# Optimization experiments

Hardware: AMD Instinct MI355X
Metric: run time of the kernel (lower is better)

Reference implementation:

```python
import jax, jax.numpy as jnp
import numpy as np

N_NODES = 50000
N_EDGES = 800000
IN_C, HID_C, OUT_C = 128, 96, 64
BN_EPS = 1e-5


def setup_inputs() -> dict:
    key = jax.random.key(0)
    ks = jax.random.split(key, 12)
    x = jax.random.normal(ks[0], (N_NODES, IN_C), dtype=jnp.float32)
    edge_weight = jax.random.uniform(ks[1], (N_EDGES,), dtype=jnp.float32)
    row = jax.random.randint(ks[2], (N_EDGES,), 0, N_NODES, dtype=jnp.int32)
    col = jax.random.randint(ks[3], (N_EDGES,), 0, N_NODES, dtype=jnp.int32)
    s = 0.05
    W1 = jax.random.normal(ks[4], (IN_C, HID_C), dtype=jnp.float32) * s
    b1 = jnp.zeros((HID_C,), dtype=jnp.float32)
    W2 = jax.random.normal(ks[5], (HID_C, HID_C), dtype=jnp.float32) * s
    b2 = jnp.zeros((HID_C,), dtype=jnp.float32)
    W3 = jax.random.normal(ks[6], (HID_C, OUT_C), dtype=jnp.float32) * s
    b3 = jnp.zeros((OUT_C,), dtype=jnp.float32)
    g1 = jnp.ones((HID_C,), dtype=jnp.float32)
    be1 = jnp.zeros((HID_C,), dtype=jnp.float32)
    g2 = jnp.ones((HID_C,), dtype=jnp.float32)
    be2 = jnp.zeros((HID_C,), dtype=jnp.float32)
    return {"x": x, "edge_weight": edge_weight, "row": row, "col": col,
            "W1": W1, "b1": b1, "W2": W2, "b2": b2, "W3": W3, "b3": b3,
            "g1": g1, "be1": be1, "g2": g2, "be2": be2}


def _gcn_conv(h, edge_weight, row, col, W, b):
    # GCNConv: adj_norm @ (h @ W) + b, adj in COO with normalized edge_weight
    h = h @ W  # [N, d_out]
    msg = edge_weight[:, None] * h[col]  # gather + scale: [E, d_out]
    agg = jax.ops.segment_sum(msg, row, num_segments=N_NODES)  # scatter-add
    return agg + b


def _batch_norm(h, gamma, beta):
    # BatchNorm1d (training-mode batch statistics, biased variance)
    mean = jnp.mean(h, axis=0)
    var = jnp.var(h, axis=0)
    return (h - mean) * jax.lax.rsqrt(var + BN_EPS) * gamma + beta


def reference(x, edge_weight, row, col, W1, b1, W2, b2, W3, b3, g1, be1, g2, be2):
    h = _gcn_conv(x, edge_weight, row, col, W1, b1)
    h = jax.nn.relu(_batch_norm(h, g1, be1))  # dropout is identity in eval
    h = _gcn_conv(h, edge_weight, row, col, W2, b2)
    h = jax.nn.relu(_batch_norm(h, g2, be2))
    h = _gcn_conv(h, edge_weight, row, col, W3, b3)
    return jax.nn.log_softmax(h, axis=-1)
```

## Files before the change

kernel.cpp:

```cpp
#include <hip/hip_runtime.h>
#include <hip/hip_bf16.h>
#include <math.h>

#define N_NODES 50000
#define N_EDGES 800000
#define IN_C 128
#define HID_C 96
#define OUT_C 64
#define BN_EPS 1e-5f

#define ELL_SHIFT 6
#define ELL_CAP   64

#define NGRP 8
#define GRP_ROWS ((N_NODES + NGRP - 1) / NGRP)

#define EW_SCALE 65535.0f
#define EW_INV   (1.0f / 65535.0f)

#define ST_SLICES 4

typedef __attribute__((ext_vector_type(8))) short short8;
typedef __attribute__((ext_vector_type(4))) float f32x4;

static __device__ __forceinline__ unsigned short f2b(float f) {
    __hip_bfloat16 b = __float2bfloat16(f);
    return *reinterpret_cast<unsigned short*>(&b);
}
static __device__ __forceinline__ float b2f(unsigned short u) {
    return __uint_as_float((unsigned)u << 16);
}
static __device__ __forceinline__ unsigned pack2(float a, float b) {
    return (unsigned)f2b(a) | ((unsigned)f2b(b) << 16);
}

#define FMA8(B, V, W)                                          \
    acc[(B) + 0] += (W) * __uint_as_float((V).x << 16);        \
    acc[(B) + 1] += (W) * __uint_as_float((V).x & 0xffff0000u);\
    acc[(B) + 2] += (W) * __uint_as_float((V).y << 16);        \
    acc[(B) + 3] += (W) * __uint_as_float((V).y & 0xffff0000u);\
    acc[(B) + 4] += (W) * __uint_as_float((V).z << 16);        \
    acc[(B) + 5] += (W) * __uint_as_float((V).z & 0xffff0000u);\
    acc[(B) + 6] += (W) * __uint_as_float((V).w << 16);        \
    acc[(B) + 7] += (W) * __uint_as_float((V).w & 0xffff0000u);

#define FMA4(B, V, W)                                          \
    acc[(B) + 0] += (W) * __uint_as_float((V).x << 16);        \
    acc[(B) + 1] += (W) * __uint_as_float((V).x & 0xffff0000u);\
    acc[(B) + 2] += (W) * __uint_as_float((V).y << 16);        \
    acc[(B) + 3] += (W) * __uint_as_float((V).y & 0xffff0000u);

__global__ void prep_all(const float* __restrict__ W1, const float* __restrict__ W2,
                         const float* __restrict__ W3,
                         unsigned short* __restrict__ Wt1,
                         unsigned short* __restrict__ Wt2,
                         unsigned short* __restrict__ Wt3,
                         int* __restrict__ cnt, float* __restrict__ stats) {
    int i = blockIdx.x * blockDim.x + threadIdx.x;
    const int n1 = IN_C * HID_C, n2 = HID_C * HID_C, n3 = HID_C * OUT_C;
    if (i < n1) {
        int j = i / IN_C, k = i % IN_C;
        Wt1[i] = f2b(W1[k * HID_C + j]);
    } else if (i < n1 + n2) {
        int t = i - n1, j = t / HID_C, k = t % HID_C;
        Wt2[t] = f2b(W2[k * HID_C + j]);
    } else if (i < n1 + n2 + n3) {
        int t = i - n1 - n2, j = t / HID_C, k = t % HID_C;
        Wt3[t] = f2b(W3[k * OUT_C + j]);
    }
    if (i < N_NODES) cnt[i] = 0;
    if (i < 2 * ST_SLICES * 2 * HID_C) stats[i] = 0.f;
}

__global__ __launch_bounds__(256)
void fill_ell(const int* __restrict__ row, const int* __restrict__ col,
              const float* __restrict__ ew, int* __restrict__ cnt,
              unsigned int* __restrict__ pairs) {
    int g = blockIdx.x & (NGRP - 1);
    int e = (blockIdx.x >> 3) * 256 + threadIdx.x;
    if (e >= N_EDGES) return;
    int r = row[e];
    int lo = g * GRP_ROWS;
    if ((unsigned)(r - lo) >= (unsigned)GRP_ROWS) return;
    int slot = atomicAdd(&cnt[r], 1);
    if (slot < ELL_CAP) {
        unsigned wq = (unsigned)(ew[e] * EW_SCALE + 0.5f);
        pairs[((size_t)r << ELL_SHIFT) + slot] = (wq << 16) | (unsigned)col[e];
    }
}

template <int K, int J, bool APPLY, bool XBF16>
__global__ __launch_bounds__(256)
void gemm_mfma(const void* __restrict__ xin,
               const unsigned short* __restrict__ Wt,
               const float* __restrict__ stats,
               const float* __restrict__ gamma,
               const float* __restrict__ beta,
               unsigned short* __restrict__ h, int N) {
    constexpr int MT = 64;
    constexpr int SK = K + 8;
    constexpr int NT = J / 16;
    __shared__ unsigned short Xs[MT * SK];
    __shared__ unsigned short Ws[J * SK];
    __shared__ float scsh_s[APPLY ? 2 * K : 2];

    int tid = threadIdx.x;
    int tileBase = blockIdx.x * MT;

    if (APPLY) {
        if (tid < K) {
            float s = 0.f, sq = 0.f;
#pragma unroll
            for (int sl = 0; sl < ST_SLICES; ++sl) {
                s  += stats[sl * 2 * K + tid];
                sq += stats[sl * 2 * K + K + tid];
            }
            const float invN = 1.f / N_NODES;
            float mean = s * invN;
            float var = sq * invN - mean * mean;
            float sc = gamma[tid] * rsqrtf(var + BN_EPS);
            scsh_s[tid] = sc;
            scsh_s[K + tid] = beta[tid] - mean * sc;
        }
        __syncthreads();
    }

    if (XBF16) {
        const unsigned short* xb = (const unsigned short*)xin;
        for (int i = tid; i < MT * (K / 8); i += 256) {
            int node = i / (K / 8), kq = i % (K / 8);
            int gn = min(tileBase + node, N - 1);
            const unsigned short* src = xb + (size_t)gn * K + kq * 8;
            ushort4 u0 = *(const ushort4*)(src);
            ushort4 u1 = *(const ushort4*)(src + 4);
            if (APPLY) {
                int kb = kq * 8;
                float v0 = fmaxf(b2f(u0.x) * scsh_s[kb + 0] + scsh_s[K + kb + 0], 0.f);
                float v1 = fmaxf(b2f(u0.y) * scsh_s[kb + 1] + scsh_s[K + kb + 1], 0.f);
                float v2 = fmaxf(b2f(u0.z) * scsh_s[kb + 2] + scsh_s[K + kb + 2], 0.f);
                float v3 = fmaxf(b2f(u0.w) * scsh_s[kb + 3] + scsh_s[K + kb + 3], 0.f);
                float v4 = fmaxf(b2f(u1.x) * scsh_s[kb + 4] + scsh_s[K + kb + 4], 0.f);
                float v5 = fmaxf(b2f(u1.y) * scsh_s[kb + 5] + scsh_s[K + kb + 5], 0.f);
                float v6 = fmaxf(b2f(u1.z) * scsh_s[kb + 6] + scsh_s[K + kb + 6], 0.f);
                float v7 = fmaxf(b2f(u1.w) * scsh_s[kb + 7] + scsh_s[K + kb + 7], 0.f);
                u0 = make_ushort4(f2b(v0), f2b(v1), f2b(v2), f2b(v3));
                u1 = make_ushort4(f2b(v4), f2b(v5), f2b(v6), f2b(v7));
            }
            *(ushort4*)&Xs[node * SK + kq * 8] = u0;
            *(ushort4*)&Xs[node * SK + kq * 8 + 4] = u1;
        }
    } else {
        const float* xf = (const float*)xin;
        for (int i = tid; i < MT * (K / 4); i += 256) {
            int node = i / (K / 4), kq = i % (K / 4);
            int gn = min(tileBase + node, N - 1);
            float4 v = *(const float4*)(xf + (size_t)gn * K + kq * 4);
            ushort4 o = make_ushort4(f2b(v.x), f2b(v.y), f2b(v.z), f2b(v.w));
            *(ushort4*)&Xs[node * SK + kq * 4] = o;
        }
    }
    for (int i = tid; i < J * (K / 4); i += 256) {
        int j = i / (K / 4), kq = i % (K / 4);
        *(ushort4*)&Ws[j * SK + kq * 4] =
            *(const ushort4*)(Wt + (size_t)j * K + kq * 4);
    }
    __syncthreads();

    int lane = tid & 63;
    int w = tid >> 6;
    int m16 = lane & 15;
    int quad = lane >> 4;

    f32x4 acc[NT];
#pragma unroll
    for (int nt = 0; nt < NT; ++nt) acc[nt] = (f32x4){0.f, 0.f, 0.f, 0.f};

    const unsigned short* xrow = &Xs[(w * 16 + m16) * SK];
#pragma unroll
    for (int k0 = 0; k0 < K; k0 += 32) {
        short8 a = *(const short8*)(xrow + k0 + quad * 8);
#pragma unroll
        for (int nt = 0; nt < NT; ++nt) {
            short8 b = *(const short8*)&Ws[(nt * 16 + m16) * SK + k0 + quad * 8];
            acc[nt] = __builtin_amdgcn_mfma_f32_16x16x32_bf16(a, b, acc[nt], 0, 0, 0);
        }
    }

#pragma unroll
    for (int nt = 0; nt < NT; ++nt) {
#pragma unroll
        for (int r = 0; r < 4; ++r) {
            int node = tileBase + w * 16 + quad * 4 + r;
            if (node < N)
                h[(size_t)node * J + nt * 16 + m16] = f2b(acc[nt][r]);
        }
    }
}

__global__ __launch_bounds__(256)
void agg96(const unsigned short* __restrict__ h,
           const int* __restrict__ cnt,
           const unsigned int* __restrict__ pairs,
           unsigned short* __restrict__ outb,
           float* __restrict__ stats) {
    constexpr int D = HID_C, C = 12;
    int tid = threadIdx.x;
    int q = tid & 7;
    int nloc = tid >> 3;
    int n = blockIdx.x * 32 + nloc;
    bool valid = n < N_NODES;
    int nn = valid ? n : N_NODES - 1;
    int end = valid ? min(cnt[nn], ELL_CAP) : 0;
    const unsigned* ep = pairs + ((size_t)nn << ELL_SHIFT);
    const int cbase = q * C;

    float acc[C];
#pragma unroll
    for (int c = 0; c < C; ++c) acc[c] = 0.f;

    int i = 0;
    for (; i + 3 < end; i += 4) {
        uint4 p = *(const uint4*)(ep + i);
        float w0 = (float)(p.x >> 16) * EW_INV;
        float w1 = (float)(p.y >> 16) * EW_INV;
        float w2 = (float)(p.z >> 16) * EW_INV;
        float w3 = (float)(p.w >> 16) * EW_INV;
        const unsigned short* r0 = h + (size_t)(p.x & 0xFFFFu) * D + cbase;
        const unsigned short* r1 = h + (size_t)(p.y & 0xFFFFu) * D + cbase;
        const unsigned short* r2 = h + (size_t)(p.z & 0xFFFFu) * D + cbase;
        const unsigned short* r3 = h + (size_t)(p.w & 0xFFFFu) * D + cbase;
        uint2 a0 = *(const uint2*)(r0), a1 = *(const uint2*)(r0 + 4), a2 = *(const uint2*)(r0 + 8);
        uint2 b0 = *(const uint2*)(r1), b1 = *(const uint2*)(r1 + 4), b2 = *(const uint2*)(r1 + 8);
        uint2 c0 = *(const uint2*)(r2), c1 = *(const uint2*)(r2 + 4), c2 = *(const uint2*)(r2 + 8);
        uint2 d0 = *(const uint2*)(r3), d1 = *(const uint2*)(r3 + 4), d2 = *(const uint2*)(r3 + 8);
        FMA4(0, a0, w0) FMA4(4, a1, w0) FMA4(8, a2, w0)
        FMA4(0, b0, w1) FMA4(4, b1, w1) FMA4(8, b2, w1)
        FMA4(0, c0, w2) FMA4(4, c1, w2) FMA4(8, c2, w2)
        FMA4(0, d0, w3) FMA4(4, d1, w3) FMA4(8, d2, w3)
    }
    for (; i < end; ++i) {
        unsigned p = ep[i];
        float w = (float)(p >> 16) * EW_INV;
        const unsigned short* r0 = h + (size_t)(p & 0xFFFFu) * D + cbase;
        uint2 a0 = *(const uint2*)(r0), a1 = *(const uint2*)(r0 + 4), a2 = *(const uint2*)(r0 + 8);
        FMA4(0, a0, w) FMA4(4, a1, w) FMA4(8, a2, w)
    }

#pragma unroll
    for (int c = 0; c < C; ++c) acc[c] = b2f(f2b(acc[c]));

    if (valid) {
        unsigned short* dst = outb + (size_t)n * D + cbase;
        uint2 o0, o1, o2;
        o0.x = pack2(acc[0], acc[1]);   o0.y = pack2(acc[2], acc[3]);
        o1.x = pack2(acc[4], acc[5]);   o1.y = pack2(acc[6], acc[7]);
        o2.x = pack2(acc[8], acc[9]);   o2.y = pack2(acc[10], acc[11]);
        *(uint2*)(dst) = o0; *(uint2*)(dst + 4) = o1; *(uint2*)(dst + 8) = o2;
    }

    __shared__ float shS[4 * 8 * C];
    __shared__ float shQ[4 * 8 * C];
    int lane = tid & 63, wv = tid >> 6;
#pragma unroll
    for (int c = 0; c < C; ++c) {
        float s = acc[c];
        float sq = s * s;
        s  += __shfl_xor(s, 8);  sq += __shfl_xor(sq, 8);
        s  += __shfl_xor(s, 16); sq += __shfl_xor(sq, 16);
        s  += __shfl_xor(s, 32); sq += __shfl_xor(sq, 32);
        if (lane < 8) { shS[(wv * 8 + lane) * C + c] = s;
                        shQ[(wv * 8 + lane) * C + c] = sq; }
    }
    __syncthreads();
    if (tid < D) {
        int qq = tid / C, cl = tid % C;
        float S = 0.f, Q = 0.f;
#pragma unroll
        for (int w2 = 0; w2 < 4; ++w2) {
            S += shS[(w2 * 8 + qq) * C + cl];
            Q += shQ[(w2 * 8 + qq) * C + cl];
        }
        int sl = blockIdx.x & (ST_SLICES - 1);
        atomicAdd(&stats[sl * 2 * D + tid], S);
        atomicAdd(&stats[sl * 2 * D + D + tid], Q);
    }
}

__global__ __launch_bounds__(256)
void agg64_lsm(const unsigned short* __restrict__ h,
               const int* __restrict__ cnt,
               const unsigned int* __restrict__ pairs,
               float* __restrict__ outf,
               const float* __restrict__ b3) {
    constexpr int D = OUT_C, C = 8;
    int tid = threadIdx.x;
    int q = tid & 7;
    int nloc = tid >> 3;
    int n = blockIdx.x * 32 + nloc;
    bool valid = n < N_NODES;
    int nn = valid ? n : N_NODES - 1;
    int end = valid ? min(cnt[nn], ELL_CAP) : 0;
    const unsigned* ep = pairs + ((size_t)nn << ELL_SHIFT);
    const int cbase = q * C;

    float acc[C];
#pragma unroll
    for (int c = 0; c < C; ++c) acc[c] = 0.f;

    int i = 0;
    for (; i + 3 < end; i += 4) {
        uint4 p = *(const uint4*)(ep + i);
        float w0 = (float)(p.x >> 16) * EW_INV;
        float w1 = (float)(p.y >> 16) * EW_INV;
        float w2 = (float)(p.z >> 16) * EW_INV;
        float w3 = (float)(p.w >> 16) * EW_INV;
        uint4 v0 = *(const uint4*)(h + (size_t)(p.x & 0xFFFFu) * D + cbase);
        uint4 v1 = *(const uint4*)(h + (size_t)(p.y & 0xFFFFu) * D + cbase);
        uint4 v2 = *(const uint4*)(h + (size_t)(p.z & 0xFFFFu) * D + cbase);
        uint4 v3 = *(const uint4*)(h + (size_t)(p.w & 0xFFFFu) * D + cbase);
        FMA8(0, v0, w0)
        FMA8(0, v1, w1)
        FMA8(0, v2, w2)
        FMA8(0, v3, w3)
    }
    for (; i < end; ++i) {
        unsigned p = ep[i];
        float w = (float)(p >> 16) * EW_INV;
        uint4 v = *(const uint4*)(h + (size_t)(p & 0xFFFFu) * D + cbase);
        FMA8(0, v, w)
    }

    float v[C];
#pragma unroll
    for (int c = 0; c < C; ++c) v[c] = acc[c] + b3[cbase + c];
    float m = v[0];
#pragma unroll
    for (int c = 1; c < C; ++c) m = fmaxf(m, v[c]);
    m = fmaxf(m, __shfl_xor(m, 1));
    m = fmaxf(m, __shfl_xor(m, 2));
    m = fmaxf(m, __shfl_xor(m, 4));
    float s = 0.f;
#pragma unroll
    for (int c = 0; c < C; ++c) s += expf(v[c] - m);
    s += __shfl_xor(s, 1);
    s += __shfl_xor(s, 2);
    s += __shfl_xor(s, 4);
    float l = m + logf(s);
    if (valid) {
        float4 o0 = make_float4(v[0] - l, v[1] - l, v[2] - l, v[3] - l);
        float4 o1 = make_float4(v[4] - l, v[5] - l, v[6] - l, v[7] - l);
        float* dst = outf + (size_t)n * D + cbase;
        *(float4*)(dst) = o0;
        *(float4*)(dst + 4) = o1;
    }
}

extern "C" void kernel_launch(void* const* d_in, const int* in_sizes, int n_in,
                              void* d_out, int out_size, void* d_ws, size_t ws_size,
                              hipStream_t stream) {
    const float* x   = (const float*)d_in[0];
    const float* ew  = (const float*)d_in[1];
    const int*   row = (const int*)d_in[2];
    const int*   col = (const int*)d_in[3];
    const float* W1  = (const float*)d_in[4];
    const float* W2  = (const float*)d_in[6];
    const float* W3  = (const float*)d_in[8];
    const float* b3  = (const float*)d_in[9];
    const float* g1  = (const float*)d_in[10];
    const float* be1 = (const float*)d_in[11];
    const float* g2  = (const float*)d_in[12];
    const float* be2 = (const float*)d_in[13];
    float* out = (float*)d_out;

    unsigned short* B      = (unsigned short*)d_ws;
    unsigned short* A      = B + (size_t)N_NODES * HID_C;
    unsigned short* Wt1    = A + (size_t)N_NODES * HID_C;
    unsigned short* Wt2    = Wt1 + IN_C * HID_C;
    unsigned short* Wt3    = Wt2 + HID_C * HID_C;
    unsigned int*   pairs  = (unsigned int*)(Wt3 + HID_C * OUT_C);
    int*            cnt    = (int*)(pairs + ((size_t)N_NODES << ELL_SHIFT));
    float*          stats1 = (float*)(cnt + N_NODES);
    float*          stats2 = stats1 + ST_SLICES * 2 * HID_C;

    const int T = 256;
    const int gridE  = (N_EDGES + T - 1) / T;
    const int gridG  = (N_NODES + 63) / 64;
    const int gridA  = (N_NODES + 31) / 32;
    const int gridP  = (N_NODES + T - 1) / T;

    prep_all<<<gridP, T, 0, stream>>>(W1, W2, W3, Wt1, Wt2, Wt3, cnt, stats1);
    fill_ell<<<gridE * NGRP, T, 0, stream>>>(row, col, ew, cnt, pairs);

    gemm_mfma<IN_C, HID_C, false, false><<<gridG, T, 0, stream>>>(
        x, Wt1, nullptr, nullptr, nullptr, A, N_NODES);
    agg96<<<gridA, T, 0, stream>>>(A, cnt, pairs, B, stats1);

    gemm_mfma<HID_C, HID_C, true, true><<<gridG, T, 0, stream>>>(
        B, Wt2, stats1, g1, be1, A, N_NODES);
    agg96<<<gridA, T, 0, stream>>>(A, cnt, pairs, B, stats2);

    gemm_mfma<HID_C, OUT_C, true, true><<<gridG, T, 0, stream>>>(
        B, Wt3, stats2, g2, be2, A, N_NODES);
    agg64_lsm<<<gridA, T, 0, stream>>>(A, cnt, pairs, out, b3);
}
```

Measured before the change: 256.6 us.

## Split each node's edge list across two thread groups in aggregation kernels

```diff
diff --git a/kernel.cpp b/kernel.cpp
--- a/kernel.cpp
+++ b/kernel.cpp
@@ -206,11 +206,15 @@
     constexpr int D = HID_C, C = 12;
     int tid = threadIdx.x;
     int q = tid & 7;
-    int nloc = tid >> 3;
-    int n = blockIdx.x * 32 + nloc;
+    int par = (tid >> 3) & 1;
+    int nloc = tid >> 4;
+    int n = blockIdx.x * 16 + nloc;
     bool valid = n < N_NODES;
     int nn = valid ? n : N_NODES - 1;
     int end = valid ? min(cnt[nn], ELL_CAP) : 0;
+    int ha = (end + 1) >> 1;
+    int lo = par ? ha : 0;
+    int hi = par ? end : ha;
     const unsigned* ep = pairs + ((size_t)nn << ELL_SHIFT);
     const int cbase = q * C;
 
@@ -218,17 +222,20 @@
 #pragma unroll
     for (int c = 0; c < C; ++c) acc[c] = 0.f;
 
-    int i = 0;
-    for (; i + 3 < end; i += 4) {
-        uint4 p = *(const uint4*)(ep + i);
-        float w0 = (float)(p.x >> 16) * EW_INV;
-        float w1 = (float)(p.y >> 16) * EW_INV;
-        float w2 = (float)(p.z >> 16) * EW_INV;
-        float w3 = (float)(p.w >> 16) * EW_INV;
-        const unsigned short* r0 = h + (size_t)(p.x & 0xFFFFu) * D + cbase;
-        const unsigned short* r1 = h + (size_t)(p.y & 0xFFFFu) * D + cbase;
-        const unsigned short* r2 = h + (size_t)(p.z & 0xFFFFu) * D + cbase;
-        const unsigned short* r3 = h + (size_t)(p.w & 0xFFFFu) * D + cbase;
+    int i = lo;
+    for (; i + 3 < hi; i += 4) {
+        unsigned p0 = __builtin_nontemporal_load(ep + i);
+        unsigned p1 = __builtin_nontemporal_load(ep + i + 1);
+        unsigned p2 = __builtin_nontemporal_load(ep + i + 2);
+        unsigned p3 = __builtin_nontemporal_load(ep + i + 3);
+        float w0 = (float)(p0 >> 16) * EW_INV;
+        float w1 = (float)(p1 >> 16) * EW_INV;
+        float w2 = (float)(p2 >> 16) * EW_INV;
+        float w3 = (float)(p3 >> 16) * EW_INV;
+        const unsigned short* r0 = h + (size_t)(p0 & 0xFFFFu) * D + cbase;
+        const unsigned short* r1 = h + (size_t)(p1 & 0xFFFFu) * D + cbase;
+        const unsigned short* r2 = h + (size_t)(p2 & 0xFFFFu) * D + cbase;
+        const unsigned short* r3 = h + (size_t)(p3 & 0xFFFFu) * D + cbase;
         uint2 a0 = *(const uint2*)(r0), a1 = *(const uint2*)(r0 + 4), a2 = *(const uint2*)(r0 + 8);
         uint2 b0 = *(const uint2*)(r1), b1 = *(const uint2*)(r1 + 4), b2 = *(const uint2*)(r1 + 8);
         uint2 c0 = *(const uint2*)(r2), c1 = *(const uint2*)(r2 + 4), c2 = *(const uint2*)(r2 + 8);
@@ -238,8 +245,8 @@
         FMA4(0, c0, w2) FMA4(4, c1, w2) FMA4(8, c2, w2)
         FMA4(0, d0, w3) FMA4(4, d1, w3) FMA4(8, d2, w3)
     }
-    for (; i < end; ++i) {
-        unsigned p = ep[i];
+    for (; i < hi; ++i) {
+        unsigned p = __builtin_nontemporal_load(ep + i);
         float w = (float)(p >> 16) * EW_INV;
         const unsigned short* r0 = h + (size_t)(p & 0xFFFFu) * D + cbase;
         uint2 a0 = *(const uint2*)(r0), a1 = *(const uint2*)(r0 + 4), a2 = *(const uint2*)(r0 + 8);
@@ -247,9 +254,12 @@
     }
 
 #pragma unroll
-    for (int c = 0; c < C; ++c) acc[c] = b2f(f2b(acc[c]));
-
-    if (valid) {
+    for (int c = 0; c < C; ++c) {
+        acc[c] += __shfl_xor(acc[c], 8);
+        acc[c] = b2f(f2b(acc[c]));
+    }
+
+    if (valid && par == 0) {
         unsigned short* dst = outb + (size_t)n * D + cbase;
         uint2 o0, o1, o2;
         o0.x = pack2(acc[0], acc[1]);   o0.y = pack2(acc[2], acc[3]);
@@ -265,7 +275,6 @@
     for (int c = 0; c < C; ++c) {
         float s = acc[c];
         float sq = s * s;
-        s  += __shfl_xor(s, 8);  sq += __shfl_xor(sq, 8);
         s  += __shfl_xor(s, 16); sq += __shfl_xor(sq, 16);
         s  += __shfl_xor(s, 32); sq += __shfl_xor(sq, 32);
         if (lane < 8) { shS[(wv * 8 + lane) * C + c] = s;
@@ -295,11 +304,15 @@
     constexpr int D = OUT_C, C = 8;
     int tid = threadIdx.x;
     int q = tid & 7;
-    int nloc = tid >> 3;
-    int n = blockIdx.x * 32 + nloc;
+    int par = (tid >> 3) & 1;
+    int nloc = tid >> 4;
+    int n = blockIdx.x * 16 + nloc;
     bool valid = n < N_NODES;
     int nn = valid ? n : N_NODES - 1;
     int end = valid ? min(cnt[nn], ELL_CAP) : 0;
+    int ha = (end + 1) >> 1;
+    int lo = par ? ha : 0;
+    int hi = par ? end : ha;
     const unsigned* ep = pairs + ((size_t)nn << ELL_SHIFT);
     const int cbase = q * C;
 
@@ -307,28 +320,34 @@
 #pragma unroll
     for (int c = 0; c < C; ++c) acc[c] = 0.f;
 
-    int i = 0;
-    for (; i + 3 < end; i += 4) {
-        uint4 p = *(const uint4*)(ep + i);
-        float w0 = (float)(p.x >> 16) * EW_INV;
-        float w1 = (float)(p.y >> 16) * EW_INV;
-        float w2 = (float)(p.z >> 16) * EW_INV;
-        float w3 = (float)(p.w >> 16) * EW_INV;
-        uint4 v0 = *(const uint4*)(h + (size_t)(p.x & 0xFFFFu) * D + cbase);
-        uint4 v1 = *(const uint4*)(h + (size_t)(p.y & 0xFFFFu) * D + cbase);
-        uint4 v2 = *(const uint4*)(h + (size_t)(p.z & 0xFFFFu) * D + cbase);
-        uint4 v3 = *(const uint4*)(h + (size_t)(p.w & 0xFFFFu) * D + cbase);
+    int i = lo;
+    for (; i + 3 < hi; i += 4) {
+        unsigned p0 = __builtin_nontemporal_load(ep + i);
+        unsigned p1 = __builtin_nontemporal_load(ep + i + 1);
+        unsigned p2 = __builtin_nontemporal_load(ep + i + 2);
+        unsigned p3 = __builtin_nontemporal_load(ep + i + 3);
+        float w0 = (float)(p0 >> 16) * EW_INV;
+        float w1 = (float)(p1 >> 16) * EW_INV;
+        float w2 = (float)(p2 >> 16) * EW_INV;
+        float w3 = (float)(p3 >> 16) * EW_INV;
+        uint4 v0 = *(const uint4*)(h + (size_t)(p0 & 0xFFFFu) * D + cbase);
+        uint4 v1 = *(const uint4*)(h + (size_t)(p1 & 0xFFFFu) * D + cbase);
+        uint4 v2 = *(const uint4*)(h + (size_t)(p2 & 0xFFFFu) * D + cbase);
+        uint4 v3 = *(const uint4*)(h + (size_t)(p3 & 0xFFFFu) * D + cbase);
         FMA8(0, v0, w0)
         FMA8(0, v1, w1)
         FMA8(0, v2, w2)
         FMA8(0, v3, w3)
     }
-    for (; i < end; ++i) {
-        unsigned p = ep[i];
+    for (; i < hi; ++i) {
+        unsigned p = __builtin_nontemporal_load(ep + i);
         float w = (float)(p >> 16) * EW_INV;
         uint4 v = *(const uint4*)(h + (size_t)(p & 0xFFFFu) * D + cbase);
         FMA8(0, v, w)
     }
+
+#pragma unroll
+    for (int c = 0; c < C; ++c) acc[c] += __shfl_xor(acc[c], 8);
 
     float v[C];
 #pragma unroll
@@ -346,7 +365,7 @@
     s += __shfl_xor(s, 2);
     s += __shfl_xor(s, 4);
     float l = m + logf(s);
-    if (valid) {
+    if (valid && par == 0) {
         float4 o0 = make_float4(v[0] - l, v[1] - l, v[2] - l, v[3] - l);
         float4 o1 = make_float4(v[4] - l, v[5] - l, v[6] - l, v[7] - l);
         float* dst = outf + (size_t)n * D + cbase;
@@ -385,7 +404,7 @@
     const int T = 256;
     const int gridE  = (N_EDGES + T - 1) / T;
     const int gridG  = (N_NODES + 63) / 64;
-    const int gridA  = (N_NODES + 31) / 32;
+    const int gridA  = (N_NODES + 15) / 16;
     const int gridP  = (N_NODES + T - 1) / T;
 
     prep_all<<<gridP, T, 0, stream>>>(W1, W2, W3, Wt1, Wt2, Wt3, cnt, stats1);
```

Result: slower. 271.6 us (+5.9%).
